# Performance work log

Measured on AMD Instinct MI355X. Metric: run time of the kernel, lower is better.

## Reference

```python
import jax, jax.numpy as jnp
import numpy as np

HEADS = 8
DIM_HEAD = 64
RADIUS = 0.2
NSAMPLE = 8
EPS = 1e-5


def setup_inputs() -> dict:
    key = jax.random.key(0)
    ks = jax.random.split(key, 6)
    b, l, n, dim = 2, 4, 1024, 512
    inner = HEADS * DIM_HEAD
    xyzs = jax.random.uniform(ks[0], (b, l, n, 3), jnp.float32)
    feature = jax.random.normal(ks[1], (b, l, n, dim), jnp.float32)
    gamma = jnp.ones((dim,), jnp.float32)
    beta = jnp.zeros((dim,), jnp.float32)
    w_qkv = jax.random.normal(ks[2], (dim, 3 * inner), jnp.float32) * 0.02
    w_spatial = jax.random.normal(ks[3], (3, DIM_HEAD), jnp.float32) * 0.02
    w_out = jax.random.normal(ks[4], (inner, dim), jnp.float32) * 0.02
    b_out = jnp.zeros((dim,), jnp.float32)
    return {"xyzs": xyzs, "feature": feature, "gamma": gamma, "beta": beta,
            "w_qkv": w_qkv, "w_spatial": w_spatial, "w_out": w_out, "b_out": b_out}


def ball_query(ref, query):
    """pointnet2-style ball query. ref:(B,N,3), query:(B,M,3) -> (B,M,NSAMPLE) int32.
    Takes the first (lowest-index) NSAMPLE in-radius points, pads with the first
    found index; all-zeros if no point is in radius (matches CUDA kernel)."""
    d2 = jnp.sum((query[:, :, None, :] - ref[:, None, :, :]) ** 2, axis=-1)  # (B,M,N)
    mask = d2 < RADIUS ** 2
    nref = ref.shape[1]
    score = jnp.where(mask, -jnp.arange(nref, dtype=jnp.float32), -jnp.inf)
    vals, pos = jax.lax.top_k(score, NSAMPLE)  # smallest in-radius indices first
    valid = vals > -jnp.inf
    first = jnp.where(valid[..., :1], pos[..., :1], 0)
    return jnp.where(valid, pos, first)


def _forward(xyzs, feature, gamma, beta, w_qkv, w_spatial, w_out, b_out):
    b, l, n, dim = feature.shape
    h, dh = HEADS, DIM_HEAD
    inner = h * dh
    scale = dh ** -0.5
    # LayerNorm over channel dim
    mu = jnp.mean(feature, -1, keepdims=True)
    var = jnp.var(feature, -1, keepdims=True)
    normf = (feature - mu) * jax.lax.rsqrt(var + EPS) * gamma + beta
    qkv = normf @ w_qkv
    q, k, v = jnp.split(qkv, 3, axis=-1)          # each (b, l, n, inner)
    xyz_flat = xyzs.reshape(b * l, n, 3)
    k_flat = k.reshape(b * l, n, inner)
    v_flat = v.reshape(b * l, n, inner)
    bidx = jnp.arange(b * l)[:, None, None]

    def per_frame(q_i, xyz_i):
        # q_i: (b, n, inner) queries of frame i; xyz_i: (b, n, 3)
        # frame-i points query neighbors inside every frame of the video
        qxyz = jnp.broadcast_to(xyz_i[:, None], (b, l, n, 3)).reshape(b * l, n, 3)
        idx = ball_query(xyz_flat, qxyz)           # (b*l, n, 8)
        g_k = k_flat[bidx, idx]                    # (b*l, n, 8, inner)
        g_v = v_flat[bidx, idx]
        g_xyz = xyz_flat[bidx, idx]                # (b*l, n, 8, 3)
        disp = g_xyz - qxyz[:, :, None]            # (b*l, n, 8, 3)
        # '(b l) n k (h d) -> b n h (l k) d'
        keys = g_k.reshape(b, l, n, NSAMPLE, h, dh).transpose(0, 2, 4, 1, 3, 5).reshape(b, n, h, l * NSAMPLE, dh)
        vals = g_v.reshape(b, l, n, NSAMPLE, h, dh).transpose(0, 2, 4, 1, 3, 5).reshape(b, n, h, l * NSAMPLE, dh)
        qh = q_i.reshape(b, n, h, dh)
        logits = jnp.einsum('bnhd,bnhjd->bnhj', qh, keys) * scale
        attn = jax.nn.softmax(logits, axis=-1)     # (b, n, h, l*8)
        # 'b l n k d -> b n (l k) d'
        dis = disp.reshape(b, l, n, NSAMPLE, 3).transpose(0, 2, 1, 3, 4).reshape(b, n, l * NSAMPLE, 3)
        dis_attn = jnp.max(attn[..., None] * dis[:, :, None], axis=3)  # (b, n, h, 3)
        dis_attn = (dis_attn @ w_spatial).reshape(b, n, inner)         # spatial_op
        attnout = jnp.einsum('bnhj,bnhjd->bnhd', attn, vals).reshape(b, n, inner)
        return attnout + dis_attn

    q_frames = jnp.moveaxis(q, 1, 0)               # (l, b, n, inner)
    xyz_frames = jnp.moveaxis(xyzs, 1, 0)          # (l, b, n, 3)
    frames = jax.vmap(per_frame)(q_frames, xyz_frames)   # (l, b, n, inner)
    frame_result = jnp.moveaxis(frames, 0, 1)      # (b, l, n, inner)
    out = jax.nn.gelu(frame_result @ w_out + b_out, approximate=False)
    return out + feature


def reference(xyzs, feature, gamma, beta, w_qkv, w_spatial, w_out, b_out):
    return _forward(xyzs, feature, gamma, beta, w_qkv, w_spatial, w_out, b_out)
```

## Files before the change

### kernel.cpp

```cpp
#include <hip/hip_runtime.h>
#include <hip/hip_bf16.h>

#define B_ 2
#define L_ 4
#define N_ 1024
#define DIM_ 512
#define INNER_ 512
#define HEADS_ 8
#define DH_ 64
#define NS_ 8
#define NFR_ (B_ * L_)
#define ROWS_ (B_ * L_ * N_)

typedef unsigned short u16;
typedef __attribute__((ext_vector_type(8))) short bf16x8;
typedef __attribute__((ext_vector_type(4))) float f32x4;

__device__ inline float bf2f(u16 u) {
    union { unsigned i; float f; } c; c.i = ((unsigned)u) << 16; return c.f;
}
__device__ inline float bflo(unsigned v) {
    union { unsigned i; float f; } c; c.i = v << 16; return c.f;
}
__device__ inline float bfhi(unsigned v) {
    union { unsigned i; float f; } c; c.i = v & 0xffff0000u; return c.f;
}
__device__ inline u16 f2bf(float x) {
    __hip_bfloat16 h = __float2bfloat16(x);
    return *reinterpret_cast<u16*>(&h);
}

#if __has_builtin(__builtin_amdgcn_fdot2_f32_bf16)
typedef __bf16 bf2v __attribute__((ext_vector_type(2)));
__device__ inline float dot8(bf16x8 a, bf16x8 b, float acc) {
    union U { bf16x8 v; bf2v p[4]; };
    U ua, ub; ua.v = a; ub.v = b;
    #pragma unroll
    for (int i = 0; i < 4; ++i)
        acc = __builtin_amdgcn_fdot2_f32_bf16(ua.p[i], ub.p[i], acc, false);
    return acc;
}
#else
__device__ inline float dot8(bf16x8 a, bf16x8 b, float acc) {
    #pragma unroll
    for (int e = 0; e < 8; ++e) acc += bf2f((u16)a[e]) * bf2f((u16)b[e]);
    return acc;
}
#endif

__global__ __launch_bounds__(256) void transpose_cvt(
    const float* __restrict__ wqkv, const float* __restrict__ wout,
    u16* __restrict__ wqkvT, u16* __restrict__ woutT)
{
    const float* src; u16* dst; int R, C, tr, tc;
    int b = blockIdx.x;
    if (b < 192) { src = wqkv; dst = wqkvT; R = 512; C = 1536; tr = b / 24; tc = b % 24; }
    else { b -= 192; src = wout; dst = woutT; R = 512; C = 512; tr = b / 8; tc = b % 8; }
    int r0 = tr * 64, c0 = tc * 64;
    int t = threadIdx.x;

    __shared__ float tile[64][65];

    int rr = t >> 2, cs = (t & 3) * 16;
    const float* sp = src + (size_t)(r0 + rr) * C + c0 + cs;
    #pragma unroll
    for (int e = 0; e < 16; e += 4) {
        f32x4 v = *(const f32x4*)(sp + e);
        tile[rr][cs + e + 0] = v[0];
        tile[rr][cs + e + 1] = v[1];
        tile[rr][cs + e + 2] = v[2];
        tile[rr][cs + e + 3] = v[3];
    }
    __syncthreads();

    int c = t >> 2, ks = (t & 3) * 16;
    u16 outv[16];
    #pragma unroll
    for (int e = 0; e < 16; ++e) outv[e] = f2bf(tile[ks + e][c]);
    u16* dp = dst + (size_t)(c0 + c) * R + r0 + ks;
    *(bf16x8*)(dp)     = *(bf16x8*)&outv[0];
    *(bf16x8*)(dp + 8) = *(bf16x8*)&outv[8];
}

__global__ __launch_bounds__(256) void ln_kernel(
    const float* __restrict__ f, const float* __restrict__ g,
    const float* __restrict__ b, u16* __restrict__ o)
{
    int row = blockIdx.x;
    int t = threadIdx.x;
    const float* fr = f + (size_t)row * DIM_;
    float x0 = fr[t], x1 = fr[t + 256];

    __shared__ float red[4];
    float s = x0 + x1;
    #pragma unroll
    for (int off = 32; off; off >>= 1) s += __shfl_xor(s, off, 64);
    if ((t & 63) == 0) red[t >> 6] = s;
    __syncthreads();
    float mu = (red[0] + red[1] + red[2] + red[3]) * (1.0f / 512.0f);
    __syncthreads();

    float d0 = x0 - mu, d1 = x1 - mu;
    float q = d0 * d0 + d1 * d1;
    #pragma unroll
    for (int off = 32; off; off >>= 1) q += __shfl_xor(q, off, 64);
    if ((t & 63) == 0) red[t >> 6] = q;
    __syncthreads();
    float var = (red[0] + red[1] + red[2] + red[3]) * (1.0f / 512.0f);
    float inv = rsqrtf(var + 1e-5f);

    o[(size_t)row * DIM_ + t]       = f2bf(d0 * inv * g[t]       + b[t]);
    o[(size_t)row * DIM_ + t + 256] = f2bf(d1 * inv * g[t + 256] + b[t + 256]);
}

__global__ __launch_bounds__(256) void gemm_bt(
    const u16* __restrict__ A, const u16* __restrict__ Bt,
    u16* __restrict__ Cb16, float* __restrict__ Cf32,
    int M, int N, int K, int nb128, int mode,
    const float* __restrict__ bias, const float* __restrict__ resid)
{
    __shared__ u16 As[128 * 40];
    __shared__ u16 Bs[128 * 40];

    int bx = blockIdx.x % nb128;
    int by = blockIdx.x / nb128;
    int m0 = by * 128, n0 = bx * 128;
    int t = threadIdx.x;
    int wave = t >> 6, lane = t & 63;
    int lr = lane & 15, quad = lane >> 4;
    int wm = (wave >> 1) * 64, wn = (wave & 1) * 64;

    f32x4 acc[4][4];
    #pragma unroll
    for (int i = 0; i < 4; ++i)
        #pragma unroll
        for (int j = 0; j < 4; ++j)
            acc[i][j] = {0.f, 0.f, 0.f, 0.f};

    for (int k0 = 0; k0 < K; k0 += 32) {
        #pragma unroll
        for (int p = 0; p < 2; ++p) {
            int c = t + p * 256;
            int r = c >> 2;
            int kc = (c & 3) * 8;
            *(bf16x8*)&As[r * 40 + kc] = *(const bf16x8*)(A + (size_t)(m0 + r) * K + k0 + kc);
            *(bf16x8*)&Bs[r * 40 + kc] = *(const bf16x8*)(Bt + (size_t)(n0 + r) * K + k0 + kc);
        }
        __syncthreads();

        bf16x8 af[4], bfr[4];
        #pragma unroll
        for (int mb = 0; mb < 4; ++mb)
            af[mb] = *(const bf16x8*)&As[(wm + mb * 16 + lr) * 40 + quad * 8];
        #pragma unroll
        for (int nb = 0; nb < 4; ++nb)
            bfr[nb] = *(const bf16x8*)&Bs[(wn + nb * 16 + lr) * 40 + quad * 8];
        #pragma unroll
        for (int mb = 0; mb < 4; ++mb)
            #pragma unroll
            for (int nb = 0; nb < 4; ++nb)
                acc[mb][nb] = __builtin_amdgcn_mfma_f32_16x16x32_bf16(
                    af[mb], bfr[nb], acc[mb][nb], 0, 0, 0);
        __syncthreads();
    }

    #pragma unroll
    for (int mb = 0; mb < 4; ++mb) {
        #pragma unroll
        for (int nb = 0; nb < 4; ++nb) {
            int col = n0 + wn + nb * 16 + lr;
            #pragma unroll
            for (int r = 0; r < 4; ++r) {
                int row = m0 + wm + mb * 16 + quad * 4 + r;
                float x = acc[mb][nb][r];
                if (mode == 1) {
                    x += bias[col];
                    float gl = 0.5f * x * (1.0f + erff(x * 0.70710678118654752f));
                    Cf32[(size_t)row * N + col] = gl + resid[(size_t)row * N + col];
                } else {
                    Cb16[(size_t)row * N + col] = f2bf(x);
                }
            }
        }
    }
}

#define RPAD_(r) ((r) + ((r) >> 4))

__global__ __launch_bounds__(256) void ballq_kernel(
    const float* __restrict__ xyz, int* __restrict__ idxt)
{
    #pragma clang fp contract(off)
    int chunk = blockIdx.x & 255;
    int combo = blockIdx.x >> 8;
    int jf = combo & 3;
    int bi = combo >> 2;

    __shared__ float rx[N_ + (N_ >> 4)], ry[N_ + (N_ >> 4)], rz[N_ + (N_ >> 4)];
    const float* ref = xyz + (size_t)((bi * L_ + jf) * N_) * 3;
    for (int p = threadIdx.x; p < N_; p += 256) {
        rx[RPAD_(p)] = ref[p * 3 + 0];
        ry[RPAD_(p)] = ref[p * 3 + 1];
        rz[RPAD_(p)] = ref[p * 3 + 2];
    }
    __syncthreads();

    int wave = threadIdx.x >> 6;
    int lane = threadIdx.x & 63;
    int n = chunk * 4 + wave;
    int base = lane * 17;
    int r0 = lane * 16;

    for (int qi = 0; qi < L_; ++qi) {
        const float* qp = xyz + (size_t)((bi * L_ + qi) * N_ + n) * 3;
        float qx = qp[0], qy = qp[1], qz = qp[2];

        unsigned mask = 0;
        #pragma unroll
        for (int j = 0; j < 16; ++j) {
            float dx = qx - rx[base + j];
            float dy = qy - ry[base + j];
            float dz = qz - rz[base + j];
            float d2 = dx * dx + dy * dy;
            d2 = d2 + dz * dz;
            if (d2 < 0.04f) mask |= (1u << j);
        }

        int cnt = __popc(mask);
        int x = cnt;
        #pragma unroll
        for (int off = 1; off < 64; off <<= 1) {
            int y = __shfl_up(x, off, 64);
            if (lane >= off) x += y;
        }
        int pre = x - cnt;
        int total = __shfl(x, 63, 64);

        int localFirst = mask ? (r0 + __builtin_ctz(mask)) : 0x7fffffff;
        int gfirst = localFirst;
        #pragma unroll
        for (int off = 32; off; off >>= 1) gfirst = min(gfirst, __shfl_xor(gfirst, off, 64));

        int* o = idxt + ((size_t)((qi * B_ + bi) * N_ + n)) * 32 + jf * NS_;

        unsigned m = mask;
        int pos = pre;
        while (m && pos < NS_) {
            int j = __builtin_ctz(m);
            o[pos] = r0 + j;
            m &= m - 1;
            ++pos;
        }
        if (lane == 0) {
            int padv = (total > 0) ? gfirst : 0;
            for (int s = (total < NS_ ? total : NS_); s < NS_; ++s) o[s] = padv;
        }
    }
}

__global__ __launch_bounds__(256, 4) void attn_kernel(
    const float* __restrict__ xyz, const u16* __restrict__ qkv,
    const int* __restrict__ idxt, const float* __restrict__ wsp,
    u16* __restrict__ fres)
{
    int x = blockIdx.x & 7;
    int bi = x >> 2;
    int qi = x & 3;
    int n = blockIdx.x >> 3;

    int wave = threadIdx.x >> 6;
    int lane = threadIdx.x & 63;
    int hh = lane >> 5;
    int j = lane & 31;
    int h = wave * 2 + hh;
    int jf = j >> 3;

    int qrow = (bi * L_ + qi) * N_ + n;
    int qq = (qi * B_ + bi) * N_ + n;

    __shared__ float a_s[HEADS_][32];
    __shared__ int grow_s[32];
    __shared__ float da_s[HEADS_][3];

    int idx = idxt[(size_t)qq * 32 + j];
    int kr = (bi * L_ + jf) * N_ + idx;

    const u16* qp = qkv + (size_t)qrow * 1536 + h * 64;
    const u16* kp = qkv + (size_t)kr * 1536 + 512 + h * 64;
    bf16x8 qv[8], kv[8];
    #pragma unroll
    for (int c = 0; c < 8; ++c) {
        kv[c] = *(const bf16x8*)(kp + c * 8);
        qv[c] = *(const bf16x8*)(qp + c * 8);
    }
    float nx = xyz[(size_t)kr * 3 + 0];
    float ny = xyz[(size_t)kr * 3 + 1];
    float nz = xyz[(size_t)kr * 3 + 2];
    __builtin_amdgcn_sched_barrier(0);

    float acc = 0.f;
    #pragma unroll
    for (int c = 0; c < 8; ++c) acc = dot8(kv[c], qv[c], acc);
    float lg = acc * 0.125f;

    float mx = lg;
    #pragma unroll
    for (int off = 16; off; off >>= 1) mx = fmaxf(mx, __shfl_xor(mx, off, 64));
    float e = expf(lg - mx);
    float sum = e;
    #pragma unroll
    for (int off = 16; off; off >>= 1) sum += __shfl_xor(sum, off, 64);
    float a = e / sum;
    a_s[h][j] = a;
    if (wave == 0 && hh == 0) grow_s[j] = kr;

    float qx = xyz[(size_t)qrow * 3 + 0];
    float qy = xyz[(size_t)qrow * 3 + 1];
    float qz = xyz[(size_t)qrow * 3 + 2];
    float tx = a * (nx - qx);
    float ty = a * (ny - qy);
    float tz = a * (nz - qz);
    #pragma unroll
    for (int off = 16; off; off >>= 1) {
        tx = fmaxf(tx, __shfl_xor(tx, off, 64));
        ty = fmaxf(ty, __shfl_xor(ty, off, 64));
        tz = fmaxf(tz, __shfl_xor(tz, off, 64));
    }
    if (j == 0) { da_s[h][0] = tx; da_s[h][1] = ty; da_s[h][2] = tz; }

    __syncthreads();

    int dd = (lane & 31) * 2;
    const u16* vbase = qkv + 1024 + h * 64 + dd;
    int rows[32];
    #pragma unroll
    for (int t = 0; t < 32; ++t) rows[t] = grow_s[t];
    unsigned vv[32];
    #pragma unroll
    for (int t = 0; t < 32; ++t)
        vv[t] = *(const unsigned*)(vbase + (size_t)rows[t] * 1536);
    __builtin_amdgcn_sched_barrier(0);

    float o0 = 0.f, o1 = 0.f;
    #pragma unroll
    for (int t = 0; t < 32; ++t) {
        float at = a_s[h][t];
        o0 += at * bflo(vv[t]);
        o1 += at * bfhi(vv[t]);
    }
    float dax = da_s[h][0], day = da_s[h][1], daz = da_s[h][2];
    float sp0 = dax * wsp[dd]     + day * wsp[64 + dd]     + daz * wsp[128 + dd];
    float sp1 = dax * wsp[dd + 1] + day * wsp[64 + dd + 1] + daz * wsp[128 + dd + 1];

    u16* op = fres + (size_t)qrow * INNER_ + h * 64 + dd;
    unsigned outw = (unsigned)f2bf(o0 + sp0) | ((unsigned)f2bf(o1 + sp1) << 16);
    *(unsigned*)op = outw;
}

extern "C" void kernel_launch(void* const* d_in, const int* in_sizes, int n_in,
                              void* d_out, int out_size, void* d_ws, size_t ws_size,
                              hipStream_t stream) {
    const float* xyz   = (const float*)d_in[0];
    const float* feat  = (const float*)d_in[1];
    const float* gamma = (const float*)d_in[2];
    const float* beta  = (const float*)d_in[3];
    const float* wqkv  = (const float*)d_in[4];
    const float* wsp   = (const float*)d_in[5];
    const float* wout  = (const float*)d_in[6];
    const float* bout  = (const float*)d_in[7];
    float* out = (float*)d_out;

    char* ws = (char*)d_ws;
    u16* normf = (u16*)ws;                 ws += (size_t)ROWS_ * DIM_ * 2;
    u16* wqkvT = (u16*)ws;                 ws += (size_t)3 * INNER_ * DIM_ * 2;
    u16* woutT = (u16*)ws;                 ws += (size_t)DIM_ * INNER_ * 2;
    u16* qkv   = (u16*)ws;                 ws += (size_t)ROWS_ * 3 * INNER_ * 2;
    int* idxt  = (int*)ws;                 ws += (size_t)L_ * NFR_ * N_ * NS_ * 4;
    u16* fres  = normf;

    transpose_cvt<<<256, 256, 0, stream>>>(wqkv, wout, wqkvT, woutT);
    ln_kernel<<<ROWS_, 256, 0, stream>>>(feat, gamma, beta, normf);
    gemm_bt<<<64 * 12, 256, 0, stream>>>(normf, wqkvT, qkv, nullptr,
                                         ROWS_, 3 * INNER_, DIM_, 12, 0, nullptr, nullptr);
    ballq_kernel<<<8 * 256, 256, 0, stream>>>(xyz, idxt);
    attn_kernel<<<ROWS_, 256, 0, stream>>>(xyz, qkv, idxt, wsp, fres);
    gemm_bt<<<64 * 4, 256, 0, stream>>>(fres, woutT, nullptr, out,
                                        ROWS_, DIM_, INNER_, 4, 1, bout, feat);
}
```

Before: 221.8 us.

## Coalesce key gathers per neighbor row and use scalar row bases in attention

The attention kernel now loads each neighbor's full key row cooperatively: each wave fetches 8 neighbor rows with one 16-byte lane load per row, and the per-head partial dots are reduced with shuffles into shared-memory logits. Before, each lane gathered 128 contiguous bytes of a single key. Neighbor indices and xyz are loaded once into shared memory, and the V gathers use readfirstlane scalar bases. The intent is fully coalesced, wider memory transactions and fewer redundant index and xyz loads, at the cost of an extra __syncthreads and shared-memory traffic.

```diff
diff --git a/kernel.cpp b/kernel.cpp
--- a/kernel.cpp
+++ b/kernel.cpp
@@ -268,41 +268,55 @@
     int qi = x & 3;
     int n = blockIdx.x >> 3;
 
-    int wave = threadIdx.x >> 6;
-    int lane = threadIdx.x & 63;
+    int t = threadIdx.x;
+    int wave = t >> 6, lane = t & 63;
+
+    int qrow = (bi * L_ + qi) * N_ + n;
+    int qq = (qi * B_ + bi) * N_ + n;
+
+    __shared__ int grow_s[32];
+    __shared__ float nx_s[32], ny_s[32], nz_s[32];
+    __shared__ float lg_s[HEADS_][33];
+    __shared__ float a_s[HEADS_][32];
+    __shared__ float da_s[HEADS_][3];
+
+    bf16x8 qf = *(const bf16x8*)(qkv + (size_t)qrow * 1536 + lane * 8);
+
+    if (t < 32) {
+        int idx = idxt[(size_t)qq * 32 + t];
+        int jf = t >> 3;
+        int kr = (bi * L_ + jf) * N_ + idx;
+        grow_s[t] = kr;
+        nx_s[t] = xyz[(size_t)kr * 3 + 0];
+        ny_s[t] = xyz[(size_t)kr * 3 + 1];
+        nz_s[t] = xyz[(size_t)kr * 3 + 2];
+    }
+    __syncthreads();
+
+    bf16x8 kf[8];
+    #pragma unroll
+    for (int r = 0; r < 8; ++r) {
+        int kr = __builtin_amdgcn_readfirstlane(grow_s[wave * 8 + r]);
+        const char* kbase = (const char*)qkv + (size_t)kr * 3072 + 1024;
+        kf[r] = *(const bf16x8*)(kbase + lane * 16);
+    }
+    __builtin_amdgcn_sched_barrier(0);
+
+    #pragma unroll
+    for (int r = 0; r < 8; ++r) {
+        float p = dot8(kf[r], qf, 0.f);
+        p += __shfl_xor(p, 1, 64);
+        p += __shfl_xor(p, 2, 64);
+        p += __shfl_xor(p, 4, 64);
+        if ((lane & 7) == 0) lg_s[lane >> 3][wave * 8 + r] = p * 0.125f;
+    }
+    __syncthreads();
+
     int hh = lane >> 5;
     int j = lane & 31;
     int h = wave * 2 + hh;
-    int jf = j >> 3;
-
-    int qrow = (bi * L_ + qi) * N_ + n;
-    int qq = (qi * B_ + bi) * N_ + n;
-
-    __shared__ float a_s[HEADS_][32];
-    __shared__ int grow_s[32];
-    __shared__ float da_s[HEADS_][3];
-
-    int idx = idxt[(size_t)qq * 32 + j];
-    int kr = (bi * L_ + jf) * N_ + idx;
-
-    const u16* qp = qkv + (size_t)qrow * 1536 + h * 64;
-    const u16* kp = qkv + (size_t)kr * 1536 + 512 + h * 64;
-    bf16x8 qv[8], kv[8];
-    #pragma unroll
-    for (int c = 0; c < 8; ++c) {
-        kv[c] = *(const bf16x8*)(kp + c * 8);
-        qv[c] = *(const bf16x8*)(qp + c * 8);
-    }
-    float nx = xyz[(size_t)kr * 3 + 0];
-    float ny = xyz[(size_t)kr * 3 + 1];
-    float nz = xyz[(size_t)kr * 3 + 2];
-    __builtin_amdgcn_sched_barrier(0);
-
-    float acc = 0.f;
-    #pragma unroll
-    for (int c = 0; c < 8; ++c) acc = dot8(kv[c], qv[c], acc);
-    float lg = acc * 0.125f;
-
+
+    float lg = lg_s[h][j];
     float mx = lg;
     #pragma unroll
     for (int off = 16; off; off >>= 1) mx = fmaxf(mx, __shfl_xor(mx, off, 64));
@@ -312,14 +326,13 @@
     for (int off = 16; off; off >>= 1) sum += __shfl_xor(sum, off, 64);
     float a = e / sum;
     a_s[h][j] = a;
-    if (wave == 0 && hh == 0) grow_s[j] = kr;
 
     float qx = xyz[(size_t)qrow * 3 + 0];
     float qy = xyz[(size_t)qrow * 3 + 1];
     float qz = xyz[(size_t)qrow * 3 + 2];
-    float tx = a * (nx - qx);
-    float ty = a * (ny - qy);
-    float tz = a * (nz - qz);
+    float tx = a * (nx_s[j] - qx);
+    float ty = a * (ny_s[j] - qy);
+    float tz = a * (nz_s[j] - qz);
     #pragma unroll
     for (int off = 16; off; off >>= 1) {
         tx = fmaxf(tx, __shfl_xor(tx, off, 64));
@@ -330,23 +343,23 @@
 
     __syncthreads();
 
-    int dd = (lane & 31) * 2;
-    const u16* vbase = qkv + 1024 + h * 64 + dd;
-    int rows[32];
-    #pragma unroll
-    for (int t = 0; t < 32; ++t) rows[t] = grow_s[t];
+    int dd = j * 2;
+    unsigned vbyte = (1024u + (unsigned)h * 64u + (unsigned)dd) * 2u;
     unsigned vv[32];
     #pragma unroll
-    for (int t = 0; t < 32; ++t)
-        vv[t] = *(const unsigned*)(vbase + (size_t)rows[t] * 1536);
+    for (int s = 0; s < 32; ++s) {
+        int r = __builtin_amdgcn_readfirstlane(grow_s[s]);
+        const char* vbase = (const char*)qkv + (size_t)r * 3072;
+        vv[s] = *(const unsigned*)(vbase + vbyte);
+    }
     __builtin_amdgcn_sched_barrier(0);
 
     float o0 = 0.f, o1 = 0.f;
     #pragma unroll
-    for (int t = 0; t < 32; ++t) {
-        float at = a_s[h][t];
-        o0 += at * bflo(vv[t]);
-        o1 += at * bfhi(vv[t]);
+    for (int s = 0; s < 32; ++s) {
+        float at = a_s[h][s];
+        o0 += at * bflo(vv[s]);
+        o1 += at * bfhi(vv[s]);
     }
     float dax = da_s[h][0], day = da_s[h][1], daz = da_s[h][2];
     float sp0 = dax * wsp[dd]     + day * wsp[64 + dd]     + daz * wsp[128 + dd];
```

Result: faster. 198.3 us (-10.6%).
